# Performance work log

Measured on AMD Instinct MI355X. Metric: run time of the kernel, lower is better.

## Reference

```python
import jax, jax.numpy as jnp
import numpy as np

B, C, IC, H, W = 2, 64, 32, 96, 96


def setup_inputs() -> dict:
    key = jax.random.key(0)
    ks = jax.random.split(key, 8)
    s_in = 1.0 / np.sqrt(C)
    s_ic = 1.0 / np.sqrt(IC)
    return {
        "x": jax.random.normal(ks[0], (B, C, H, W), dtype=jnp.float32),
        "Wg": jax.random.uniform(ks[1], (IC, C), jnp.float32, -s_in, s_in),
        "bg": jax.random.uniform(ks[2], (IC,), jnp.float32, -s_in, s_in),
        "Wt": jax.random.uniform(ks[3], (IC, C), jnp.float32, -s_in, s_in),
        "bt": jax.random.uniform(ks[4], (IC,), jnp.float32, -s_in, s_in),
        "Wp": jax.random.uniform(ks[5], (IC, C), jnp.float32, -s_in, s_in),
        "bp": jax.random.uniform(ks[6], (IC,), jnp.float32, -s_in, s_in),
        "Wo": jax.random.uniform(ks[7], (C, IC), jnp.float32, -s_ic, s_ic),
        "bo": jax.random.uniform(jax.random.fold_in(key, 9), (C,), jnp.float32, -s_ic, s_ic),
    }


def reference(x, Wg, bg, Wt, bt, Wp, bp, Wo, bo):
    b, c, h, w = x.shape
    n = h * w
    xf = x.reshape(b, c, n)  # [B, C, N]

    def proj(Wc, bc):  # 1x1 conv == channel GEMM -> [B, IC, N]
        return jnp.einsum("bcn,oc->bon", xf, Wc) + bc[None, :, None]

    g = proj(Wg, bg)
    theta = proj(Wt, bt)
    phi = proj(Wp, bp)
    scores = jnp.einsum("bcn,bcm->bnm", theta, phi)  # [B, N, N]
    att = jax.nn.softmax(scores, axis=-1)
    y = jnp.einsum("bnm,bcm->bcn", att, g)  # [B, IC, N]
    o = jnp.einsum("bcn,oc->bon", y, Wo) + bo[None, :, None]  # [B, C, N]
    return o.reshape(b, c, h, w) + x
```

## Files before the change

### kernel.cpp

```cpp
#include <hip/hip_runtime.h>
#include <hip/hip_bf16.h>


#define B_   2
#define C_   64
#define IC_  32
#define N_   9216
#define SEG_       8
#define SEG_KEYS   1152
#define SEG_TILES  18
#define QBLK128    72
#define LOG2E 1.44269504088896f

typedef __attribute__((ext_vector_type(4))) float  f32x4;
typedef __attribute__((ext_vector_type(8))) short  s16x8;
typedef __attribute__((ext_vector_type(4))) short  s16x4;

static __device__ __forceinline__ ushort f2bf(float f) {
  union { __hip_bfloat16 h; ushort u; } cv;
  cv.h = __float2bfloat16(f);
  return cv.u;
}

static __device__ __forceinline__ float bf2f(ushort u) {
  union { uint i; float f; } c;
  c.i = ((uint)u) << 16;
  return c.f;
}

static __device__ __forceinline__ f32x4 mfma32(s16x8 a, s16x8 b, f32x4 c) {
  return __builtin_amdgcn_mfma_f32_16x16x32_bf16(a, b, c, 0, 0, 0);
}

__global__ __launch_bounds__(256) void proj_kernel(
    const float* __restrict__ x,
    const float* __restrict__ Wg, const float* __restrict__ bg,
    const float* __restrict__ Wt, const float* __restrict__ bt,
    const float* __restrict__ Wp, const float* __restrict__ bp,
    ushort* __restrict__ Qb, ushort* __restrict__ Kb, ushort* __restrict__ Vt)
{
  const int grp = blockIdx.x / 72;
  const int ic0 = grp * 8;
  const int bn  = (blockIdx.x % 72) * 256 + threadIdx.x;
  const int b   = bn / N_;
  const int n   = bn % N_;

  float ag[8], at_[8], ap[8];
#pragma unroll
  for (int j = 0; j < 8; ++j) { ag[j] = 0.f; at_[j] = 0.f; ap[j] = 0.f; }

  const float* xp = x + (size_t)b * C_ * N_ + n;
#pragma unroll 8
  for (int c = 0; c < C_; ++c) {
    const float xv = xp[(size_t)c * N_];
#pragma unroll
    for (int j = 0; j < 8; ++j) {
      ag[j]  = fmaf(Wg[(ic0 + j) * C_ + c], xv, ag[j]);
      at_[j] = fmaf(Wt[(ic0 + j) * C_ + c], xv, at_[j]);
      ap[j]  = fmaf(Wp[(ic0 + j) * C_ + c], xv, ap[j]);
    }
  }

  const int j6 = n & 63, u = j6 >> 5, r = j6 & 31;
  const int nperm = (n - j6) + u * 32 + (r & 15) * 2 + (r >> 4);

#pragma unroll
  for (int j = 0; j < 8; ++j) {
    const int ic = ic0 + j;
    Qb[(size_t)bn * IC_ + ic] = f2bf(LOG2E * (at_[j] + bt[ic]));
    Kb[(size_t)bn * IC_ + ic] = f2bf(ap[j] + bp[ic]);
    Vt[(size_t)(b * IC_ + ic) * N_ + nperm] = f2bf(ag[j] + bg[ic]);
  }
}

__global__ __launch_bounds__(256, 4) void attn_kernel(
    const ushort* __restrict__ Qb, const ushort* __restrict__ Kb,
    const ushort* __restrict__ Vt, ushort* __restrict__ Opart,
    float* __restrict__ Lp)
{
  __shared__ __align__(16) ushort Kl[64 * 40];
  __shared__ __align__(16) ushort Vl[32 * 70];

  const int qblk = blockIdx.x % QBLK128;
  const int bs   = blockIdx.x / QBLK128;
  const int seg  = bs & (SEG_ - 1);
  const int b    = bs >> 3;
  const int key0 = seg * SEG_KEYS;

  const int tid  = threadIdx.x;
  const int lane = tid & 63;
  const int wave = tid >> 6;
  const int q16  = lane & 15;
  const int h    = lane >> 4;

  const int qbaseA = qblk * 128 + wave * 32;
  const int qbaseB = qbaseA + 16;

  const short ONE = (short)0x3F80;
  const s16x8 ones = {ONE, ONE, ONE, ONE, ONE, ONE, ONE, ONE};

  const s16x8 qfragA = *reinterpret_cast<const s16x8*>(
      Qb + (size_t)(b * N_ + qbaseA + q16) * IC_ + h * 8);
  const s16x8 qfragB = *reinterpret_cast<const s16x8*>(
      Qb + (size_t)(b * N_ + qbaseB + q16) * IC_ + h * 8);

  f32x4 aA0 = {0.f,0.f,0.f,0.f}, aA1 = {0.f,0.f,0.f,0.f}, aLA = {0.f,0.f,0.f,0.f};
  f32x4 aB0 = {0.f,0.f,0.f,0.f}, aB1 = {0.f,0.f,0.f,0.f}, aLB = {0.f,0.f,0.f,0.f};

  const int krow = tid >> 2, kpart = tid & 3;
  const ushort* kg = Kb + ((size_t)b * N_ + key0 + krow) * IC_ + kpart * 8;
  ushort* kl_dst = &Kl[krow * 40 + kpart * 8];

  const int vd = tid >> 3, vp = tid & 7;
  const ushort* vg = Vt + (size_t)(b * IC_ + vd) * N_ + key0 + vp * 8;
  ushort* vl_dst = &Vl[vd * 70 + vp * 8];

  s16x8 kreg = *reinterpret_cast<const s16x8*>(kg);
  s16x8 vreg = *reinterpret_cast<const s16x8*>(vg);

  for (int it = 0; it < SEG_TILES; ++it) {
    *reinterpret_cast<s16x8*>(kl_dst) = kreg;
    *reinterpret_cast<s16x8*>(vl_dst) = vreg;
    __syncthreads();

    if (it + 1 < SEG_TILES) {
      kg += 64 * IC_;
      vg += 64;
      kreg = *reinterpret_cast<const s16x8*>(kg);
      vreg = *reinterpret_cast<const s16x8*>(vg);
    }

#pragma unroll
    for (int u = 0; u < 2; ++u) {
      const s16x8 kf0 = *reinterpret_cast<const s16x8*>(&Kl[(u * 32 + q16) * 40 + h * 8]);
      const s16x8 kf1 = *reinterpret_cast<const s16x8*>(&Kl[(u * 32 + 16 + q16) * 40 + h * 8]);
      const f32x4 z = {0.f, 0.f, 0.f, 0.f};
      const f32x4 sA0 = mfma32(kf0, qfragA, z);
      const f32x4 sA1 = mfma32(kf1, qfragA, z);
      const f32x4 sB0 = mfma32(kf0, qfragB, z);
      const f32x4 sB1 = mfma32(kf1, qfragB, z);

      const s16x8 vf0 = *reinterpret_cast<const s16x8*>(&Vl[q16 * 70 + u * 32 + h * 8]);
      const s16x8 vf1 = *reinterpret_cast<const s16x8*>(&Vl[(16 + q16) * 70 + u * 32 + h * 8]);

      union { ushort us[8]; s16x8 v; } paA, paB;
#pragma unroll
      for (int i = 0; i < 4; ++i) {
        paA.us[2 * i]     = f2bf(__builtin_amdgcn_exp2f(sA0[i]));
        paA.us[2 * i + 1] = f2bf(__builtin_amdgcn_exp2f(sA1[i]));
        paB.us[2 * i]     = f2bf(__builtin_amdgcn_exp2f(sB0[i]));
        paB.us[2 * i + 1] = f2bf(__builtin_amdgcn_exp2f(sB1[i]));
      }
      aA0 = mfma32(paA.v, vf0, aA0);
      aA1 = mfma32(paA.v, vf1, aA1);
      aLA = mfma32(paA.v, ones, aLA);
      aB0 = mfma32(paB.v, vf0, aB0);
      aB1 = mfma32(paB.v, vf1, aB1);
      aLB = mfma32(paB.v, ones, aLB);
    }
    __syncthreads();
  }

  const size_t obase0 = ((size_t)(b * SEG_ + seg) * N_);
#pragma unroll
  for (int r = 0; r < 4; ++r) {
    const int qA = qbaseA + h * 4 + r;
    const int qB = qbaseB + h * 4 + r;
    Opart[(obase0 + qA) * IC_ + q16]      = f2bf(aA0[r]);
    Opart[(obase0 + qA) * IC_ + 16 + q16] = f2bf(aA1[r]);
    Opart[(obase0 + qB) * IC_ + q16]      = f2bf(aB0[r]);
    Opart[(obase0 + qB) * IC_ + 16 + q16] = f2bf(aB1[r]);
  }
  if (q16 == 0) {
#pragma unroll
    for (int r = 0; r < 4; ++r) {
      Lp[obase0 + qbaseA + h * 4 + r] = aLA[r];
      Lp[obase0 + qbaseB + h * 4 + r] = aLB[r];
    }
  }
}

__global__ __launch_bounds__(256) void combine_kernel(
    const ushort* __restrict__ Opart, const float* __restrict__ Lp,
    float* __restrict__ Y)
{
  const int idx     = blockIdx.x * 256 + threadIdx.x;
  const int bn      = idx >> 2;
  const int quarter = idx & 3;
  const int b       = bn / N_;
  const int q       = bn % N_;

  float l = 0.f;
  float o[8];
#pragma unroll
  for (int j = 0; j < 8; ++j) o[j] = 0.f;

#pragma unroll
  for (int s = 0; s < SEG_; ++s) {
    const size_t base = (size_t)(b * SEG_ + s) * N_ + q;
    l += Lp[base];
    union { s16x8 v; ushort us[8]; } ov;
    ov.v = *reinterpret_cast<const s16x8*>(Opart + base * IC_ + quarter * 8);
#pragma unroll
    for (int j = 0; j < 8; ++j) o[j] += bf2f(ov.us[j]);
  }
  const float inv = 1.0f / l;
  f32x4 y0 = {o[0] * inv, o[1] * inv, o[2] * inv, o[3] * inv};
  f32x4 y1 = {o[4] * inv, o[5] * inv, o[6] * inv, o[7] * inv};
  f32x4* yp = reinterpret_cast<f32x4*>(Y + (size_t)bn * IC_ + quarter * 8);
  yp[0] = y0; yp[1] = y1;
}

__global__ __launch_bounds__(256) void out_kernel(
    const float* __restrict__ Y, const float* __restrict__ Wo,
    const float* __restrict__ bo, const float* __restrict__ x,
    float* __restrict__ out)
{
  const int g    = blockIdx.x / 72;
  const int oc0  = g * 16;
  const int bn   = (blockIdx.x % 72) * 256 + threadIdx.x;
  const int b    = bn / N_;
  const int n    = bn % N_;

  float yv[32];
#pragma unroll
  for (int i = 0; i < 8; ++i) {
    const f32x4 v = *reinterpret_cast<const f32x4*>(Y + (size_t)bn * IC_ + i * 4);
    yv[i * 4 + 0] = v[0]; yv[i * 4 + 1] = v[1];
    yv[i * 4 + 2] = v[2]; yv[i * 4 + 3] = v[3];
  }

  float acc[16];
#pragma unroll
  for (int j = 0; j < 16; ++j) acc[j] = bo[oc0 + j];

#pragma unroll
  for (int ic = 0; ic < IC_; ++ic) {
    const float yv_ic = yv[ic];
#pragma unroll
    for (int j = 0; j < 16; ++j)
      acc[j] = fmaf(Wo[(oc0 + j) * IC_ + ic], yv_ic, acc[j]);
  }

#pragma unroll
  for (int j = 0; j < 16; ++j) {
    const int oc = oc0 + j;
    const size_t xi = (size_t)(b * C_ + oc) * N_ + n;
    out[xi] = acc[j] + x[xi];
  }
}

extern "C" void kernel_launch(void* const* d_in, const int* in_sizes, int n_in,
                              void* d_out, int out_size, void* d_ws, size_t ws_size,
                              hipStream_t stream)
{
  const float* x  = (const float*)d_in[0];
  const float* Wg = (const float*)d_in[1];
  const float* bg = (const float*)d_in[2];
  const float* Wt = (const float*)d_in[3];
  const float* bt = (const float*)d_in[4];
  const float* Wp = (const float*)d_in[5];
  const float* bp = (const float*)d_in[6];
  const float* Wo = (const float*)d_in[7];
  const float* bo = (const float*)d_in[8];
  float* out = (float*)d_out;

  char* ws = (char*)d_ws;
  const size_t szb  = (size_t)B_ * N_ * IC_ * sizeof(ushort);
  const size_t szOp = (size_t)B_ * SEG_ * N_ * IC_ * sizeof(ushort);
  ushort* Qb = (ushort*)(ws);
  ushort* Kb = (ushort*)(ws + szb);
  ushort* Vt = (ushort*)(ws + 2 * szb);
  ushort* Op = (ushort*)(ws + 3 * szb);
  float*  Lp = (float*)(ws + 3 * szb + szOp);
  float*  Yw = (float*)(ws);

  proj_kernel<<<288, 256, 0, stream>>>(x, Wg, bg, Wt, bt, Wp, bp, Qb, Kb, Vt);
  attn_kernel<<<B_ * SEG_ * QBLK128, 256, 0, stream>>>(Qb, Kb, Vt, Op, Lp);
  combine_kernel<<<(B_ * N_ * 4) / 256, 256, 0, stream>>>(Op, Lp, Yw);
  out_kernel<<<4 * 72, 256, 0, stream>>>(Yw, Wo, bo, x, out);
}
```

Measured before the change: 75.30 us.

## Double-buffer attention LDS, raise split-K segments, and vectorize projection stores

The attention kernel now uses double-buffered K/V tiles in shared memory, so each tile needs one barrier instead of two. It also moves to 16 key segments when the workspace allows it, raising the launch bound to 8 blocks per SM and shrinking the K stride. The projection kernel handles two positions per thread and writes Q/K as 16-byte vector stores. The intermediate Y is stored as bf16 to halve its traffic. In exchange, the combine step now reads twice as many partials, and the bf16 Y loses some precision.

New measurement: 125.6 us. 1.67x slower.

```diff
diff --git a/kernel.cpp b/kernel.cpp
--- a/kernel.cpp
+++ b/kernel.cpp
@@ -6,12 +6,10 @@
 #define C_   64
 #define IC_  32
 #define N_   9216
-#define SEG_       8
-#define SEG_KEYS   1152
-#define SEG_TILES  18
 #define QBLK128    72
 #define LOG2E 1.44269504088896f
 
+typedef __attribute__((ext_vector_type(2))) float  f32x2;
 typedef __attribute__((ext_vector_type(4))) float  f32x4;
 typedef __attribute__((ext_vector_type(8))) short  s16x8;
 typedef __attribute__((ext_vector_type(4))) short  s16x4;
@@ -39,53 +37,76 @@
     const float* __restrict__ Wp, const float* __restrict__ bp,
     ushort* __restrict__ Qb, ushort* __restrict__ Kb, ushort* __restrict__ Vt)
 {
-  const int grp = blockIdx.x / 72;
+  const int grp = blockIdx.x / 36;
   const int ic0 = grp * 8;
-  const int bn  = (blockIdx.x % 72) * 256 + threadIdx.x;
-  const int b   = bn / N_;
-  const int n   = bn % N_;
-
-  float ag[8], at_[8], ap[8];
-#pragma unroll
-  for (int j = 0; j < 8; ++j) { ag[j] = 0.f; at_[j] = 0.f; ap[j] = 0.f; }
+  const int bn0 = (blockIdx.x % 36) * 512 + threadIdx.x * 2;
+  const int b   = bn0 / N_;
+  const int n   = bn0 % N_;
+
+  float ag[8][2], at_[8][2], ap[8][2];
+#pragma unroll
+  for (int j = 0; j < 8; ++j)
+#pragma unroll
+    for (int k = 0; k < 2; ++k) { ag[j][k] = 0.f; at_[j][k] = 0.f; ap[j][k] = 0.f; }
 
   const float* xp = x + (size_t)b * C_ * N_ + n;
-#pragma unroll 8
+#pragma unroll 4
   for (int c = 0; c < C_; ++c) {
-    const float xv = xp[(size_t)c * N_];
+    const f32x2 xv = *reinterpret_cast<const f32x2*>(xp + (size_t)c * N_);
 #pragma unroll
     for (int j = 0; j < 8; ++j) {
-      ag[j]  = fmaf(Wg[(ic0 + j) * C_ + c], xv, ag[j]);
-      at_[j] = fmaf(Wt[(ic0 + j) * C_ + c], xv, at_[j]);
-      ap[j]  = fmaf(Wp[(ic0 + j) * C_ + c], xv, ap[j]);
-    }
-  }
-
-  const int j6 = n & 63, u = j6 >> 5, r = j6 & 31;
-  const int nperm = (n - j6) + u * 32 + (r & 15) * 2 + (r >> 4);
-
-#pragma unroll
-  for (int j = 0; j < 8; ++j) {
-    const int ic = ic0 + j;
-    Qb[(size_t)bn * IC_ + ic] = f2bf(LOG2E * (at_[j] + bt[ic]));
-    Kb[(size_t)bn * IC_ + ic] = f2bf(ap[j] + bp[ic]);
-    Vt[(size_t)(b * IC_ + ic) * N_ + nperm] = f2bf(ag[j] + bg[ic]);
-  }
-}
-
-__global__ __launch_bounds__(256, 4) void attn_kernel(
+      const float wg = Wg[(ic0 + j) * C_ + c];
+      const float wt = Wt[(ic0 + j) * C_ + c];
+      const float wp = Wp[(ic0 + j) * C_ + c];
+#pragma unroll
+      for (int k = 0; k < 2; ++k) {
+        ag[j][k]  = fmaf(wg, xv[k], ag[j][k]);
+        at_[j][k] = fmaf(wt, xv[k], at_[j][k]);
+        ap[j][k]  = fmaf(wp, xv[k], ap[j][k]);
+      }
+    }
+  }
+
+#pragma unroll
+  for (int k = 0; k < 2; ++k) {
+    const int bn = bn0 + k, nn = n + k;
+    union { ushort u[8]; s16x8 v; } qv, kv;
+#pragma unroll
+    for (int j = 0; j < 8; ++j) {
+      const int ic = ic0 + j;
+      qv.u[j] = f2bf(LOG2E * (at_[j][k] + bt[ic]));
+      kv.u[j] = f2bf(ap[j][k] + bp[ic]);
+    }
+    *reinterpret_cast<s16x8*>(Qb + (size_t)bn * IC_ + ic0) = qv.v;
+    *reinterpret_cast<s16x8*>(Kb + (size_t)bn * IC_ + ic0) = kv.v;
+    const int j6 = nn & 63, u = j6 >> 5, r = j6 & 31;
+    const int nperm = (nn - j6) + u * 32 + (r & 15) * 2 + (r >> 4);
+#pragma unroll
+    for (int j = 0; j < 8; ++j) {
+      const int ic = ic0 + j;
+      Vt[(size_t)(b * IC_ + ic) * N_ + nperm] = f2bf(ag[j][k] + bg[ic]);
+    }
+  }
+}
+
+template<int NSEG>
+__global__ __launch_bounds__(256, 8) void attn_kernel(
     const ushort* __restrict__ Qb, const ushort* __restrict__ Kb,
     const ushort* __restrict__ Vt, ushort* __restrict__ Opart,
     float* __restrict__ Lp)
 {
-  __shared__ __align__(16) ushort Kl[64 * 40];
-  __shared__ __align__(16) ushort Vl[32 * 70];
+  constexpr int NT = 144 / NSEG;
+  constexpr int SKEYS = N_ / NSEG;
+  constexpr int KSTR = 36;
+  constexpr int VSTR = 70;
+  __shared__ __align__(16) ushort Kl[2][64 * KSTR];
+  __shared__ __align__(16) ushort Vl[2][32 * VSTR];
 
   const int qblk = blockIdx.x % QBLK128;
   const int bs   = blockIdx.x / QBLK128;
-  const int seg  = bs & (SEG_ - 1);
-  const int b    = bs >> 3;
-  const int key0 = seg * SEG_KEYS;
+  const int seg  = bs % NSEG;
+  const int b    = bs / NSEG;
+  const int key0 = seg * SKEYS;
 
   const int tid  = threadIdx.x;
   const int lane = tid & 63;
@@ -109,39 +130,47 @@
 
   const int krow = tid >> 2, kpart = tid & 3;
   const ushort* kg = Kb + ((size_t)b * N_ + key0 + krow) * IC_ + kpart * 8;
-  ushort* kl_dst = &Kl[krow * 40 + kpart * 8];
+  const int kloff = krow * KSTR + kpart * 8;
 
   const int vd = tid >> 3, vp = tid & 7;
   const ushort* vg = Vt + (size_t)(b * IC_ + vd) * N_ + key0 + vp * 8;
-  ushort* vl_dst = &Vl[vd * 70 + vp * 8];
+  const int vloff = vd * VSTR + vp * 8;
 
   s16x8 kreg = *reinterpret_cast<const s16x8*>(kg);
   s16x8 vreg = *reinterpret_cast<const s16x8*>(vg);
-
-  for (int it = 0; it < SEG_TILES; ++it) {
-    *reinterpret_cast<s16x8*>(kl_dst) = kreg;
-    *reinterpret_cast<s16x8*>(vl_dst) = vreg;
-    __syncthreads();
-
-    if (it + 1 < SEG_TILES) {
-      kg += 64 * IC_;
-      vg += 64;
-      kreg = *reinterpret_cast<const s16x8*>(kg);
-      vreg = *reinterpret_cast<const s16x8*>(vg);
-    }
-
+  *reinterpret_cast<s16x8*>(&Kl[0][kloff]) = kreg;
+  *reinterpret_cast<s16x8*>(&Vl[0][vloff]) = vreg;
+  if (NT > 1) {
+    kreg = *reinterpret_cast<const s16x8*>(kg + (size_t)64 * IC_);
+    vreg = *reinterpret_cast<const s16x8*>(vg + 64);
+  }
+  __syncthreads();
+
+  for (int it = 0; it < NT; ++it) {
+    const int cur = it & 1, nxt = cur ^ 1;
+    if (it + 1 < NT) {
+      *reinterpret_cast<s16x8*>(&Kl[nxt][kloff]) = kreg;
+      *reinterpret_cast<s16x8*>(&Vl[nxt][vloff]) = vreg;
+    }
+    if (it + 2 < NT) {
+      kreg = *reinterpret_cast<const s16x8*>(kg + (size_t)(it + 2) * 64 * IC_);
+      vreg = *reinterpret_cast<const s16x8*>(vg + (it + 2) * 64);
+    }
+
+    const ushort* Klc = Kl[cur];
+    const ushort* Vlc = Vl[cur];
 #pragma unroll
     for (int u = 0; u < 2; ++u) {
-      const s16x8 kf0 = *reinterpret_cast<const s16x8*>(&Kl[(u * 32 + q16) * 40 + h * 8]);
-      const s16x8 kf1 = *reinterpret_cast<const s16x8*>(&Kl[(u * 32 + 16 + q16) * 40 + h * 8]);
+      const s16x8 kf0 = *reinterpret_cast<const s16x8*>(&Klc[(u * 32 + q16) * KSTR + h * 8]);
+      const s16x8 kf1 = *reinterpret_cast<const s16x8*>(&Klc[(u * 32 + 16 + q16) * KSTR + h * 8]);
       const f32x4 z = {0.f, 0.f, 0.f, 0.f};
       const f32x4 sA0 = mfma32(kf0, qfragA, z);
       const f32x4 sA1 = mfma32(kf1, qfragA, z);
       const f32x4 sB0 = mfma32(kf0, qfragB, z);
       const f32x4 sB1 = mfma32(kf1, qfragB, z);
 
-      const s16x8 vf0 = *reinterpret_cast<const s16x8*>(&Vl[q16 * 70 + u * 32 + h * 8]);
-      const s16x8 vf1 = *reinterpret_cast<const s16x8*>(&Vl[(16 + q16) * 70 + u * 32 + h * 8]);
+      const s16x8 vf0 = *reinterpret_cast<const s16x8*>(&Vlc[q16 * VSTR + u * 32 + h * 8]);
+      const s16x8 vf1 = *reinterpret_cast<const s16x8*>(&Vlc[(16 + q16) * VSTR + u * 32 + h * 8]);
 
       union { ushort us[8]; s16x8 v; } paA, paB;
 #pragma unroll
@@ -161,7 +190,7 @@
     __syncthreads();
   }
 
-  const size_t obase0 = ((size_t)(b * SEG_ + seg) * N_);
+  const size_t obase0 = ((size_t)(b * NSEG + seg) * N_);
 #pragma unroll
   for (int r = 0; r < 4; ++r) {
     const int qA = qbaseA + h * 4 + r;
@@ -180,9 +209,10 @@
   }
 }
 
+template<int NSEG>
 __global__ __launch_bounds__(256) void combine_kernel(
     const ushort* __restrict__ Opart, const float* __restrict__ Lp,
-    float* __restrict__ Y)
+    ushort* __restrict__ Y)
 {
   const int idx     = blockIdx.x * 256 + threadIdx.x;
   const int bn      = idx >> 2;
@@ -196,8 +226,8 @@
   for (int j = 0; j < 8; ++j) o[j] = 0.f;
 
 #pragma unroll
-  for (int s = 0; s < SEG_; ++s) {
-    const size_t base = (size_t)(b * SEG_ + s) * N_ + q;
+  for (int s = 0; s < NSEG; ++s) {
+    const size_t base = (size_t)(b * NSEG + s) * N_ + q;
     l += Lp[base];
     union { s16x8 v; ushort us[8]; } ov;
     ov.v = *reinterpret_cast<const s16x8*>(Opart + base * IC_ + quarter * 8);
@@ -205,14 +235,14 @@
     for (int j = 0; j < 8; ++j) o[j] += bf2f(ov.us[j]);
   }
   const float inv = 1.0f / l;
-  f32x4 y0 = {o[0] * inv, o[1] * inv, o[2] * inv, o[3] * inv};
-  f32x4 y1 = {o[4] * inv, o[5] * inv, o[6] * inv, o[7] * inv};
-  f32x4* yp = reinterpret_cast<f32x4*>(Y + (size_t)bn * IC_ + quarter * 8);
-  yp[0] = y0; yp[1] = y1;
+  union { ushort us[8]; s16x8 v; } yv;
+#pragma unroll
+  for (int j = 0; j < 8; ++j) yv.us[j] = f2bf(o[j] * inv);
+  *reinterpret_cast<s16x8*>(Y + (size_t)bn * IC_ + quarter * 8) = yv.v;
 }
 
 __global__ __launch_bounds__(256) void out_kernel(
-    const float* __restrict__ Y, const float* __restrict__ Wo,
+    const ushort* __restrict__ Y, const float* __restrict__ Wo,
     const float* __restrict__ bo, const float* __restrict__ x,
     float* __restrict__ out)
 {
@@ -224,10 +254,11 @@
 
   float yv[32];
 #pragma unroll
-  for (int i = 0; i < 8; ++i) {
-    const f32x4 v = *reinterpret_cast<const f32x4*>(Y + (size_t)bn * IC_ + i * 4);
-    yv[i * 4 + 0] = v[0]; yv[i * 4 + 1] = v[1];
-    yv[i * 4 + 2] = v[2]; yv[i * 4 + 3] = v[3];
+  for (int i = 0; i < 4; ++i) {
+    union { s16x8 v; ushort us[8]; } ov;
+    ov.v = *reinterpret_cast<const s16x8*>(Y + (size_t)bn * IC_ + i * 8);
+#pragma unroll
+    for (int j = 0; j < 8; ++j) yv[i * 8 + j] = bf2f(ov.us[j]);
   }
 
   float acc[16];
@@ -266,17 +297,24 @@
   float* out = (float*)d_out;
 
   char* ws = (char*)d_ws;
-  const size_t szb  = (size_t)B_ * N_ * IC_ * sizeof(ushort);
-  const size_t szOp = (size_t)B_ * SEG_ * N_ * IC_ * sizeof(ushort);
+  const size_t szb = (size_t)B_ * N_ * IC_ * sizeof(ushort);
   ushort* Qb = (ushort*)(ws);
   ushort* Kb = (ushort*)(ws + szb);
   ushort* Vt = (ushort*)(ws + 2 * szb);
   ushort* Op = (ushort*)(ws + 3 * szb);
-  float*  Lp = (float*)(ws + 3 * szb + szOp);
-  float*  Yw = (float*)(ws);
-
-  proj_kernel<<<288, 256, 0, stream>>>(x, Wg, bg, Wt, bt, Wp, bp, Qb, Kb, Vt);
-  attn_kernel<<<B_ * SEG_ * QBLK128, 256, 0, stream>>>(Qb, Kb, Vt, Op, Lp);
-  combine_kernel<<<(B_ * N_ * 4) / 256, 256, 0, stream>>>(Op, Lp, Yw);
-  out_kernel<<<4 * 72, 256, 0, stream>>>(Yw, Wo, bo, x, out);
-}
+  ushort* Yb = (ushort*)(ws);
+
+  const size_t need16 = 3 * szb + 16 * szb + (size_t)16 * B_ * N_ * sizeof(float);
+
+  proj_kernel<<<144, 256, 0, stream>>>(x, Wg, bg, Wt, bt, Wp, bp, Qb, Kb, Vt);
+  if (ws_size >= need16) {
+    float* Lp = (float*)(ws + 3 * szb + 16 * szb);
+    attn_kernel<16><<<B_ * 16 * QBLK128, 256, 0, stream>>>(Qb, Kb, Vt, Op, Lp);
+    combine_kernel<16><<<(B_ * N_ * 4) / 256, 256, 0, stream>>>(Op, Lp, Yb);
+  } else {
+    float* Lp = (float*)(ws + 3 * szb + 8 * szb);
+    attn_kernel<8><<<B_ * 8 * QBLK128, 256, 0, stream>>>(Qb, Kb, Vt, Op, Lp);
+    combine_kernel<8><<<(B_ * N_ * 4) / 256, 256, 0, stream>>>(Op, Lp, Yb);
+  }
+  out_kernel<<<4 * 72, 256, 0, stream>>>(Yb, Wo, bo, x, out);
+}
```
